# Optimization experiments

Measured on AMD Instinct MI355X. Metric: run time of the kernel, lower is better.

The kernel has to match this reference:

```python
import jax, jax.numpy as jnp
import numpy as np

KH = KW = 3
STRIDE, PAD, DIL = 1, 1, 1
HEADS, DG, CLIP, C = 12, 12, 2, 192
B, H, W = 4, 48, 48


def _linear_chw(x, w, b):
    # x: (n, d, c, h, w); Linear over channel dim (module rearranges to channels-last)
    return jnp.einsum('ndchw,oc->ndohw', x, w) + b[None, None, :, None, None]


def _deform_attn(q, kv, offset):
    # q: (b,1,C,H,W); kv: (b,clip,2C,H,W); offset: (b,clip,DG*K*2,H,W)
    b = q.shape[0]
    K = KH * KW
    HW = H * W
    dim = C // HEADS
    cg = 2 * C // DG  # channels per deformable group in kv (standard im2col split)
    ky = jnp.repeat(jnp.arange(KH), KW).astype(jnp.float32)  # (K,)
    kx = jnp.tile(jnp.arange(KW), KH).astype(jnp.float32)
    off = offset.reshape(b, CLIP, DG, K, 2, H, W)  # per-group [y,x] pairs per tap
    base_y = jnp.arange(H, dtype=jnp.float32)[None, :, None] * STRIDE - PAD + ky[:, None, None] * DIL  # (K,H,1)
    base_x = jnp.arange(W, dtype=jnp.float32)[None, None, :] * STRIDE - PAD + kx[:, None, None] * DIL  # (K,1,W)
    py = base_y + off[:, :, :, :, 0]  # (b,clip,dg,K,H,W)
    px = base_x + off[:, :, :, :, 1]
    kv_g = kv.reshape(b, CLIP, DG, cg, HW)

    y0 = jnp.floor(py)
    x0 = jnp.floor(px)
    wy1 = py - y0
    wx1 = px - x0

    def corner(yi, xi, wgt):
        valid = (yi >= 0) & (yi <= H - 1) & (xi >= 0) & (xi <= W - 1)
        idx = (jnp.clip(yi, 0, H - 1) * W + jnp.clip(xi, 0, W - 1)).astype(jnp.int32)
        idx = jnp.broadcast_to(idx.reshape(b, CLIP, DG, K, 1, HW), (b, CLIP, DG, K, cg, HW))
        src = jnp.broadcast_to(kv_g[:, :, :, None], (b, CLIP, DG, K, cg, HW))
        vals = jnp.take_along_axis(src, idx, axis=-1)  # gather over source pixels
        w_eff = (wgt * valid.astype(wgt.dtype)).reshape(b, CLIP, DG, K, 1, HW)
        return vals * w_eff

    s = (corner(y0, x0, (1 - wy1) * (1 - wx1))
         + corner(y0, x0 + 1, (1 - wy1) * wx1)
         + corner(y0 + 1, x0, wy1 * (1 - wx1))
         + corner(y0 + 1, x0 + 1, wy1 * wx1))  # (b,clip,dg,K,cg,HW)
    # restore channel order: (dg, cg) -> 2C = [C of k, C of v]
    s = s.transpose(0, 1, 2, 4, 3, 5).reshape(b, CLIP, 2, HEADS, dim, K, HW)
    ks, vs = s[:, :, 0], s[:, :, 1]  # (b,clip,heads,dim,K,HW)
    qh = q.reshape(b, HEADS, dim, HW) * (dim ** -0.5)
    scores = jnp.einsum('bhdn,bchdkn->bnhck', qh, ks)  # (b,HW,heads,clip,K)
    attn = jax.nn.softmax(scores.reshape(b, HW, HEADS, CLIP * K), axis=-1).reshape(b, HW, HEADS, CLIP, K)
    out = jnp.einsum('bnhck,bchdkn->bhdn', attn, vs)
    return out.reshape(b, 1, C, H, W)


def setup_inputs() -> dict:
    key = jax.random.key(0)
    ks = jax.random.split(key, 16)
    sd = 0.02
    return {
        'q': jax.random.normal(ks[0], (B, 1, C, H, W), jnp.float32),
        'k': jax.random.normal(ks[1], (B, CLIP, C, H, W), jnp.float32),
        'v': jax.random.normal(ks[2], (B, CLIP, C, H, W), jnp.float32),
        'offset': jax.random.normal(ks[3], (B, CLIP, DG * KH * KW * 2, H, W), jnp.float32),
        'wq': jax.random.normal(ks[4], (C, C), jnp.float32) * sd,
        'bq': jnp.zeros((C,), jnp.float32),
        'wk': jax.random.normal(ks[5], (C, C), jnp.float32) * sd,
        'bk': jnp.zeros((C,), jnp.float32),
        'wv': jax.random.normal(ks[6], (C, C), jnp.float32) * sd,
        'bv': jnp.zeros((C,), jnp.float32),
        'w1': jax.random.normal(ks[7], (2 * C, C), jnp.float32) * sd,
        'b1': jnp.zeros((2 * C,), jnp.float32),
        'w2': jax.random.normal(ks[8], (C, 2 * C), jnp.float32) * sd,
        'b2': jnp.zeros((C,), jnp.float32),
    }


def reference(q, k, v, offset, wq, bq, wk, bk, wv, bv, w1, b1, w2, b2):
    qp = _linear_chw(q, wq, bq)
    kv = jnp.concatenate([_linear_chw(k, wk, bk), _linear_chw(v, wv, bv)], axis=2)
    o = _deform_attn(qp, kv, offset)
    h = jnp.einsum('ndchw,oc->ndohw', o, w1) + b1[None, None, :, None, None]
    h = jax.nn.gelu(h, approximate=False)
    m = jnp.einsum('ndchw,oc->ndohw', h, w2) + b2[None, None, :, None, None]
    return o + m
```

## Files before the change

### kernel.cpp

```cpp
#include <hip/hip_runtime.h>

#define HW 2304
#define WID 48

typedef __attribute__((ext_vector_type(8))) short bf16x8;
typedef __attribute__((ext_vector_type(4))) float f32x4;
typedef __attribute__((ext_vector_type(2))) _Float16 half2v;

__device__ __forceinline__ half2v pk_h2(float lo, float hi) {
  return __builtin_bit_cast(half2v, __builtin_amdgcn_cvt_pkrtz(lo, hi));
}

__device__ __forceinline__ unsigned pack_bf2(float lo, float hi) {
  unsigned a = __builtin_bit_cast(unsigned, lo);
  unsigned b = __builtin_bit_cast(unsigned, hi);
  a = (a + 0x7FFFu + ((a >> 16) & 1u)) >> 16;
  b = (b + 0x7FFFu + ((b >> 16) & 1u)) >> 16;
  return a | (b << 16);
}
__device__ __forceinline__ unsigned short bf16_of(float x) {
  unsigned u = __builtin_bit_cast(unsigned, x);
  u = (u + 0x7FFFu + ((u >> 16) & 1u)) >> 16;
  return (unsigned short)u;
}
__device__ __forceinline__ unsigned short f16_of(float x) {
  _Float16 h = (_Float16)x;
  return __builtin_bit_cast(unsigned short, h);
}

__global__ __launch_bounds__(256) void prep_w(
    const float* __restrict__ wq, const float* __restrict__ wk,
    const float* __restrict__ wv, const float* __restrict__ w1,
    const float* __restrict__ w2, unsigned* __restrict__ wf)
{
  int fid = blockIdx.x * 4 + (threadIdx.x >> 6);
  int l = threadIdx.x & 63;
  const float* src; int K; int base;
  if (fid < 72)       { src = wq; K = 192; base = 0; }
  else if (fid < 144) { src = wk; K = 192; base = 72; }
  else if (fid < 216) { src = wv; K = 192; base = 144; }
  else if (fid < 360) { src = w1; K = 192; base = 216; }
  else                { src = w2; K = 384; base = 360; }
  int local = fid - base;
  int KS = K / 32;
  int nf = local / KS, ks = local % KS;
  int row = nf * 16 + (l & 15);
  int c0 = ks * 32 + (l >> 4) * 8;
  const float* p = src + (size_t)row * K + c0;
  float4 v0 = *(const float4*)p;
  float4 v1 = *(const float4*)(p + 4);
  unsigned* dst = wf + ((size_t)fid * 64 + l) * 4;
  dst[0] = pack_bf2(v0.x, v0.y);
  dst[1] = pack_bf2(v0.z, v0.w);
  dst[2] = pack_bf2(v1.x, v1.y);
  dst[3] = pack_bf2(v1.z, v1.w);
}

__global__ __launch_bounds__(256) void proj_mfma(
    const float* __restrict__ q, const float* __restrict__ k, const float* __restrict__ v,
    const unsigned* __restrict__ wf,
    const float* __restrict__ bq, const float* __restrict__ bk, const float* __restrict__ bv,
    float* __restrict__ qp, unsigned short* __restrict__ kvp)
{
  __shared__ unsigned lds[64 * 100];
  int slab = blockIdx.y;
  const float* in; const unsigned* wfr; const float* bias;
  float* outf = nullptr; unsigned short* outh = nullptr;
  if (slab < 4) {
    in = q + (size_t)slab * 192 * HW; wfr = wf; bias = bq;
    outf = qp + (size_t)slab * HW * 192;
  } else if (slab < 12) {
    int c = slab - 4;
    in = k + (size_t)c * 192 * HW; wfr = wf + 72 * 256; bias = bk;
    outh = kvp + (size_t)c * 2 * 6 * HW * 32;
  } else {
    int c = slab - 12;
    in = v + (size_t)c * 192 * HW; wfr = wf + 144 * 256; bias = bv;
    outh = kvp + ((size_t)c * 2 + 1) * 6 * HW * 32;
  }
  const int n0 = blockIdx.x * 64;
  const int t = threadIdx.x;
  const int w = t >> 6, l = t & 63;

  {
    int pix = t & 63;
    int cp0 = t >> 6;
    const float* s0 = in + n0 + pix;
#pragma unroll
    for (int i = 0; i < 24; ++i) {
      int cp = cp0 * 24 + i;
      float lo = s0[(size_t)(2 * cp) * HW];
      float hi = s0[(size_t)(2 * cp + 1) * HW];
      lds[pix * 100 + cp] = pack_bf2(lo, hi);
    }
  }

  bf16x8 wfrag[6][3];
#pragma unroll
  for (int ks = 0; ks < 6; ++ks)
#pragma unroll
    for (int nfi = 0; nfi < 3; ++nfi) {
      int nf = w * 3 + nfi;
      wfrag[ks][nfi] = ((const bf16x8*)wfr)[(nf * 6 + ks) * 64 + l];
    }

  __syncthreads();

  f32x4 acc[3][4];
#pragma unroll
  for (int a = 0; a < 3; ++a)
#pragma unroll
    for (int m = 0; m < 4; ++m) acc[a][m] = (f32x4){0.f, 0.f, 0.f, 0.f};

#pragma unroll
  for (int ks = 0; ks < 6; ++ks) {
    bf16x8 af[4];
#pragma unroll
    for (int mf = 0; mf < 4; ++mf)
      af[mf] = *(const bf16x8*)&lds[(mf * 16 + (l & 15)) * 100 + ks * 16 + (l >> 4) * 4];
#pragma unroll
    for (int nfi = 0; nfi < 3; ++nfi)
#pragma unroll
      for (int mf = 0; mf < 4; ++mf)
        acc[nfi][mf] = __builtin_amdgcn_mfma_f32_16x16x32_bf16(af[mf], wfrag[ks][nfi], acc[nfi][mf], 0, 0, 0);
  }

#pragma unroll
  for (int nfi = 0; nfi < 3; ++nfi) {
    int oc = (w * 3 + nfi) * 16 + (l & 15);
    float bs = bias[oc];
    if (outf) {
#pragma unroll
      for (int mf = 0; mf < 4; ++mf) {
        int pixb = n0 + mf * 16 + (l >> 4) * 4;
#pragma unroll
        for (int j = 0; j < 4; ++j)
          outf[(size_t)(pixb + j) * 192 + oc] = acc[nfi][mf][j] + bs;
      }
    } else {
      int pkh = oc >> 5, ch = oc & 31;
#pragma unroll
      for (int mf = 0; mf < 4; ++mf) {
        int pixb = n0 + mf * 16 + (l >> 4) * 4;
#pragma unroll
        for (int j = 0; j < 4; ++j)
          outh[((size_t)pkh * HW + pixb + j) * 32 + ch] = f16_of(acc[nfi][mf][j] + bs);
      }
    }
  }
}

__global__ __launch_bounds__(256, 4) void attn_kernel(
    const float* __restrict__ qp, const unsigned short* __restrict__ kvp,
    const float* __restrict__ offs, float* __restrict__ o_ws)
{
  __shared__ uint4 rec[2][2][9][32];
  const int t = threadIdx.x;
  const int g = blockIdx.x & 7;
  const int pos = blockIdx.x >> 3;
  const int b = g >> 1;
  const int half = g & 1;
  const int pk = pos / 36;
  const int tile = pos % 36;
  const int n_base = half * 1152 + tile * 32;

#pragma unroll
  for (int i = 0; i < 5; ++i) {
    int rid = t + i * 256;
    if (rid < 1152) {
      int rpix = rid & 31;
      int rest = rid >> 5;
      int rtap = rest % 9;
      int rq = rest / 9;
      int rclip = rq & 1;
      int dgsel = rq >> 1;
      int rn = n_base + rpix;
      int rh = rn / WID, rw = rn % WID;
      int dg = pk + dgsel * 6;
      const float* ob = offs + ((size_t)(b * 2 + rclip) * 216 + (size_t)(dg * 9 + rtap) * 2) * HW + rn;
      float oy = ob[0];
      float ox = ob[HW];
      float py = (float)(rh - 1 + rtap / 3) + oy;
      float px = (float)(rw - 1 + rtap % 3) + ox;
      float y0f = floorf(py), x0f = floorf(px);
      int y0 = (int)y0f, x0 = (int)x0f;
      float wy1 = py - y0f, wx1 = px - x0f;
      float wy0 = 1.f - wy1, wx0 = 1.f - wx1;
      unsigned ip[2];
      float wv[4];
#pragma unroll
      for (int cy = 0; cy < 2; ++cy) {
        int yi = y0 + cy;
        float wyv = cy ? wy1 : wy0;
        int yc = yi < 0 ? 0 : (yi > 47 ? 47 : yi);
        bool vy = (unsigned)yi < 48u;
#pragma unroll
        for (int cx = 0; cx < 2; ++cx) {
          int xi = x0 + cx;
          float wxv = cx ? wx1 : wx0;
          int xc = xi < 0 ? 0 : (xi > 47 ? 47 : xi);
          bool vx = (unsigned)xi < 48u;
          float wgt = (vy && vx) ? wyv * wxv : 0.f;
          int ci = cy * 2 + cx;
          wv[ci] = wgt;
          ((unsigned short*)ip)[ci] = (unsigned short)(yc * WID + xc);
        }
      }
      uint4 rc;
      rc.x = ip[0];
      rc.y = ip[1];
      rc.z = __builtin_bit_cast(unsigned, pk_h2(wv[0], wv[1]));
      rc.w = __builtin_bit_cast(unsigned, pk_h2(wv[2], wv[3]));
      rec[dgsel][rclip][rtap][rpix] = rc;
    }
  }

  const int l8 = t & 7;
  const int csel = l8 >> 2;
  const int chq = l8 & 3;
  const int pix = t >> 3;
  const int n = n_base + pix;

  half2v qh[4];
  {
    const float* qb = qp + ((size_t)b * HW + n) * 192 + pk * 32 + chq * 8;
    float4 v0 = *(const float4*)qb;
    float4 v1 = *(const float4*)(qb + 4);
    qh[0] = pk_h2(v0.x * 0.25f, v0.y * 0.25f);
    qh[1] = pk_h2(v0.z * 0.25f, v0.w * 0.25f);
    qh[2] = pk_h2(v1.x * 0.25f, v1.y * 0.25f);
    qh[3] = pk_h2(v1.z * 0.25f, v1.w * 0.25f);
  }

  __syncthreads();

  float sc[18];

#pragma unroll
  for (int c = 0; c < 2; ++c) {
    const unsigned short* kb = kvp + (((size_t)(b * 2 + c) * 2 + 0) * 6 + pk) * HW * 32 + chq * 8;
#pragma unroll
    for (int kk = 0; kk < 9; ++kk) {
      uint4 rc = rec[0][c][kk][pix];
      float s = 0.f;
#pragma unroll
      for (int r = 0; r < 2; ++r) {
        unsigned pr = r ? rc.y : rc.x;
        unsigned idx = csel ? (pr >> 16) : (pr & 0xFFFFu);
        half2v wp = __builtin_bit_cast(half2v, r ? rc.w : rc.z);
        _Float16 wh = csel ? wp.y : wp.x;
        uint4 u = *(const uint4*)(kb + (size_t)idx * 32);
        float d = __builtin_amdgcn_fdot2(qh[0], __builtin_bit_cast(half2v, u.x), 0.f, false);
        d = __builtin_amdgcn_fdot2(qh[1], __builtin_bit_cast(half2v, u.y), d, false);
        d = __builtin_amdgcn_fdot2(qh[2], __builtin_bit_cast(half2v, u.z), d, false);
        d = __builtin_amdgcn_fdot2(qh[3], __builtin_bit_cast(half2v, u.w), d, false);
        s += (float)wh * d;
      }
      sc[c * 9 + kk] = s;
    }
  }

#pragma unroll
  for (int j = 0; j < 18; ++j) sc[j] += __shfl_xor(sc[j], 1, 64);
#pragma unroll
  for (int j = 0; j < 18; ++j) sc[j] += __shfl_xor(sc[j], 4, 64);

  {
    float m = -1e30f;
#pragma unroll
    for (int j = 0; j < 18; ++j) m = fmaxf(m, sc[j]);
    float sum = 0.f;
#pragma unroll
    for (int j = 0; j < 18; ++j) { float ev = __expf(sc[j] - m); sc[j] = ev; sum += ev; }
    float inv = 1.f / sum;
#pragma unroll
    for (int j = 0; j < 18; ++j) sc[j] *= inv;
  }

  float acc[8];
#pragma unroll
  for (int i = 0; i < 8; ++i) acc[i] = 0.f;
#pragma unroll
  for (int c = 0; c < 2; ++c) {
    const unsigned short* vb = kvp + (((size_t)(b * 2 + c) * 2 + 1) * 6 + pk) * HW * 32 + chq * 8;
#pragma unroll
    for (int kk = 0; kk < 9; ++kk) {
      uint4 rc = rec[1][c][kk][pix];
      float at = sc[c * 9 + kk];
#pragma unroll
      for (int r = 0; r < 2; ++r) {
        unsigned pr = r ? rc.y : rc.x;
        unsigned idx = csel ? (pr >> 16) : (pr & 0xFFFFu);
        half2v wp = __builtin_bit_cast(half2v, r ? rc.w : rc.z);
        _Float16 wh = csel ? wp.y : wp.x;
        uint4 u = *(const uint4*)(vb + (size_t)idx * 32);
        float cw = (float)wh * at;
        half2v v0 = __builtin_bit_cast(half2v, u.x);
        half2v v1 = __builtin_bit_cast(half2v, u.y);
        half2v v2 = __builtin_bit_cast(half2v, u.z);
        half2v v3 = __builtin_bit_cast(half2v, u.w);
        acc[0] += cw * (float)v0.x; acc[1] += cw * (float)v0.y;
        acc[2] += cw * (float)v1.x; acc[3] += cw * (float)v1.y;
        acc[4] += cw * (float)v2.x; acc[5] += cw * (float)v2.y;
        acc[6] += cw * (float)v3.x; acc[7] += cw * (float)v3.y;
      }
    }
  }

#pragma unroll
  for (int i = 0; i < 8; ++i) acc[i] += __shfl_xor(acc[i], 4, 64);

  if (csel == 0) {
    float* orow = o_ws + ((size_t)b * HW + n) * 192 + pk * 32 + chq * 8;
    float4 r0; r0.x = acc[0]; r0.y = acc[1]; r0.z = acc[2]; r0.w = acc[3];
    float4 r1; r1.x = acc[4]; r1.y = acc[5]; r1.z = acc[6]; r1.w = acc[7];
    *(float4*)orow = r0;
    *(float4*)(orow + 4) = r1;
  }
}

__global__ __launch_bounds__(256) void mlp_mfma(
    const float* __restrict__ o_ws, const unsigned* __restrict__ wf,
    const float* __restrict__ b1, const float* __restrict__ b2,
    float* __restrict__ out)
{
  __shared__ unsigned ldsO[16 * 100];
  __shared__ unsigned ldsH[16 * 196];
  const unsigned* w1f = wf + 216 * 256;
  const unsigned* w2f = wf + 360 * 256;
  const int blk = blockIdx.x;
  const int b = blk / 144;
  const int n0 = (blk % 144) * 16;
  const int t = threadIdx.x;
  const int w = t >> 6, l = t & 63;

  for (int i = t; i < 16 * 96; i += 256) {
    int pix = i / 96, cp = i % 96;
    const float2 s = *(const float2*)(o_ws + ((size_t)(b * HW) + n0 + pix) * 192 + 2 * cp);
    ldsO[pix * 100 + cp] = pack_bf2(s.x, s.y);
  }
  __syncthreads();

  f32x4 acc1[6];
#pragma unroll
  for (int a = 0; a < 6; ++a) acc1[a] = (f32x4){0.f, 0.f, 0.f, 0.f};
#pragma unroll
  for (int ks = 0; ks < 6; ++ks) {
    bf16x8 af = *(const bf16x8*)&ldsO[(l & 15) * 100 + ks * 16 + (l >> 4) * 4];
#pragma unroll
    for (int nfi = 0; nfi < 6; ++nfi) {
      int nf = w * 6 + nfi;
      bf16x8 bfr = ((const bf16x8*)w1f)[(nf * 6 + ks) * 64 + l];
      acc1[nfi] = __builtin_amdgcn_mfma_f32_16x16x32_bf16(af, bfr, acc1[nfi], 0, 0, 0);
    }
  }

  {
    unsigned short* ldsHu = (unsigned short*)ldsH;
#pragma unroll
    for (int nfi = 0; nfi < 6; ++nfi) {
      int hc = (w * 6 + nfi) * 16 + (l & 15);
      float bs = b1[hc];
#pragma unroll
      for (int j = 0; j < 4; ++j) {
        int pix = (l >> 4) * 4 + j;
        float x = acc1[nfi][j] + bs;
        float gl = 0.5f * x * (1.f + erff(x * 0.70710678118654752f));
        ldsHu[pix * 392 + hc] = bf16_of(gl);
      }
    }
  }
  __syncthreads();

  f32x4 acc2[3];
#pragma unroll
  for (int a = 0; a < 3; ++a) acc2[a] = (f32x4){0.f, 0.f, 0.f, 0.f};
#pragma unroll
  for (int ks = 0; ks < 12; ++ks) {
    bf16x8 af = *(const bf16x8*)&ldsH[(l & 15) * 196 + ks * 16 + (l >> 4) * 4];
#pragma unroll
    for (int nfi = 0; nfi < 3; ++nfi) {
      int nf = w * 3 + nfi;
      bf16x8 bfr = ((const bf16x8*)w2f)[(nf * 12 + ks) * 64 + l];
      acc2[nfi] = __builtin_amdgcn_mfma_f32_16x16x32_bf16(af, bfr, acc2[nfi], 0, 0, 0);
    }
  }

#pragma unroll
  for (int nfi = 0; nfi < 3; ++nfi) {
    int oc = (w * 3 + nfi) * 16 + (l & 15);
    float bs = b2[oc];
#pragma unroll
    for (int j = 0; j < 4; ++j) {
      int pix = (l >> 4) * 4 + j;
      float res = o_ws[((size_t)(b * HW) + n0 + pix) * 192 + oc];
      out[((size_t)b * 192 + oc) * HW + n0 + pix] = acc2[nfi][j] + bs + res;
    }
  }
}

extern "C" void kernel_launch(void* const* d_in, const int* in_sizes, int n_in,
                              void* d_out, int out_size, void* d_ws, size_t ws_size,
                              hipStream_t stream) {
  const float* q = (const float*)d_in[0];
  const float* k = (const float*)d_in[1];
  const float* v = (const float*)d_in[2];
  const float* offset = (const float*)d_in[3];
  const float* wq = (const float*)d_in[4];
  const float* bq = (const float*)d_in[5];
  const float* wk = (const float*)d_in[6];
  const float* bk = (const float*)d_in[7];
  const float* wv = (const float*)d_in[8];
  const float* bv = (const float*)d_in[9];
  const float* w1 = (const float*)d_in[10];
  const float* b1 = (const float*)d_in[11];
  const float* w2 = (const float*)d_in[12];
  const float* b2 = (const float*)d_in[13];
  float* out = (float*)d_out;

  float* qp_t = (float*)d_ws;
  float* o_ws = qp_t + (size_t)4 * HW * 192;
  unsigned short* kvp = (unsigned short*)(o_ws + (size_t)4 * HW * 192);
  unsigned* wfb = (unsigned*)(kvp + (size_t)8 * 2 * 6 * HW * 32);

  prep_w<<<dim3(126), dim3(256), 0, stream>>>(wq, wk, wv, w1, w2, wfb);
  proj_mfma<<<dim3(36, 20), dim3(256), 0, stream>>>(q, k, v, wfb, bq, bk, bv, qp_t, kvp);
  attn_kernel<<<dim3(1728), dim3(256), 0, stream>>>(qp_t, kvp, offset, o_ws);
  mlp_mfma<<<dim3(576), dim3(256), 0, stream>>>(o_ws, wfb, b1, b2, out);
}
```

Baseline: 64.37 us.

## Split deformable attention across clips with flash-style partial softmax combine

The attention kernel now handles one clip per block, doubling the grid. Each block writes unnormalized outputs along with its running max and sum to a partial buffer. A new combine kernel merges the two clip partials using log-sum-exp rescaling and writes the normalized output. This adds parallelism and cuts per-block register and LDS use, at the cost of an extra kernel launch and a round trip of partial results through global memory.

```diff
diff --git a/kernel.cpp b/kernel.cpp
--- a/kernel.cpp
+++ b/kernel.cpp
@@ -150,34 +150,35 @@
   }
 }
 
-__global__ __launch_bounds__(256, 4) void attn_kernel(
+__global__ __launch_bounds__(256, 4) void attn_part(
     const float* __restrict__ qp, const unsigned short* __restrict__ kvp,
-    const float* __restrict__ offs, float* __restrict__ o_ws)
+    const float* __restrict__ offs, float* __restrict__ opart)
 {
-  __shared__ uint4 rec[2][2][9][32];
+  __shared__ uint4 rec[2][9][32];
   const int t = threadIdx.x;
   const int g = blockIdx.x & 7;
   const int pos = blockIdx.x >> 3;
   const int b = g >> 1;
   const int half = g & 1;
-  const int pk = pos / 36;
-  const int tile = pos % 36;
+  const int clip = pos / 216;
+  const int r2 = pos % 216;
+  const int pk = r2 / 36;
+  const int tile = r2 % 36;
   const int n_base = half * 1152 + tile * 32;
-
-#pragma unroll
-  for (int i = 0; i < 5; ++i) {
+  const int bc = b * 2 + clip;
+
+#pragma unroll
+  for (int i = 0; i < 3; ++i) {
     int rid = t + i * 256;
-    if (rid < 1152) {
+    if (rid < 576) {
       int rpix = rid & 31;
       int rest = rid >> 5;
       int rtap = rest % 9;
-      int rq = rest / 9;
-      int rclip = rq & 1;
-      int dgsel = rq >> 1;
+      int dgsel = rest / 9;
       int rn = n_base + rpix;
       int rh = rn / WID, rw = rn % WID;
       int dg = pk + dgsel * 6;
-      const float* ob = offs + ((size_t)(b * 2 + rclip) * 216 + (size_t)(dg * 9 + rtap) * 2) * HW + rn;
+      const float* ob = offs + ((size_t)bc * 216 + (size_t)(dg * 9 + rtap) * 2) * HW + rn;
       float oy = ob[0];
       float ox = ob[HW];
       float py = (float)(rh - 1 + rtap / 3) + oy;
@@ -211,7 +212,7 @@
       rc.y = ip[1];
       rc.z = __builtin_bit_cast(unsigned, pk_h2(wv[0], wv[1]));
       rc.w = __builtin_bit_cast(unsigned, pk_h2(wv[2], wv[3]));
-      rec[dgsel][rclip][rtap][rpix] = rc;
+      rec[dgsel][rtap][rpix] = rc;
     }
   }
 
@@ -234,14 +235,13 @@
 
   __syncthreads();
 
-  float sc[18];
-
-#pragma unroll
-  for (int c = 0; c < 2; ++c) {
-    const unsigned short* kb = kvp + (((size_t)(b * 2 + c) * 2 + 0) * 6 + pk) * HW * 32 + chq * 8;
+  float sc[9];
+
+  {
+    const unsigned short* kb = kvp + (((size_t)bc * 2 + 0) * 6 + pk) * HW * 32 + chq * 8;
 #pragma unroll
     for (int kk = 0; kk < 9; ++kk) {
-      uint4 rc = rec[0][c][kk][pix];
+      uint4 rc = rec[0][kk][pix];
       float s = 0.f;
 #pragma unroll
       for (int r = 0; r < 2; ++r) {
@@ -256,37 +256,31 @@
         d = __builtin_amdgcn_fdot2(qh[3], __builtin_bit_cast(half2v, u.w), d, false);
         s += (float)wh * d;
       }
-      sc[c * 9 + kk] = s;
-    }
-  }
-
-#pragma unroll
-  for (int j = 0; j < 18; ++j) sc[j] += __shfl_xor(sc[j], 1, 64);
-#pragma unroll
-  for (int j = 0; j < 18; ++j) sc[j] += __shfl_xor(sc[j], 4, 64);
-
+      sc[kk] = s;
+    }
+  }
+
+#pragma unroll
+  for (int j = 0; j < 9; ++j) sc[j] += __shfl_xor(sc[j], 1, 64);
+#pragma unroll
+  for (int j = 0; j < 9; ++j) sc[j] += __shfl_xor(sc[j], 4, 64);
+
+  float m = -1e30f;
+#pragma unroll
+  for (int j = 0; j < 9; ++j) m = fmaxf(m, sc[j]);
+  float Z = 0.f;
+#pragma unroll
+  for (int j = 0; j < 9; ++j) { float ev = __expf(sc[j] - m); sc[j] = ev; Z += ev; }
+
+  float acc[8];
+#pragma unroll
+  for (int i = 0; i < 8; ++i) acc[i] = 0.f;
   {
-    float m = -1e30f;
-#pragma unroll
-    for (int j = 0; j < 18; ++j) m = fmaxf(m, sc[j]);
-    float sum = 0.f;
-#pragma unroll
-    for (int j = 0; j < 18; ++j) { float ev = __expf(sc[j] - m); sc[j] = ev; sum += ev; }
-    float inv = 1.f / sum;
-#pragma unroll
-    for (int j = 0; j < 18; ++j) sc[j] *= inv;
-  }
-
-  float acc[8];
-#pragma unroll
-  for (int i = 0; i < 8; ++i) acc[i] = 0.f;
-#pragma unroll
-  for (int c = 0; c < 2; ++c) {
-    const unsigned short* vb = kvp + (((size_t)(b * 2 + c) * 2 + 1) * 6 + pk) * HW * 32 + chq * 8;
+    const unsigned short* vb = kvp + (((size_t)bc * 2 + 1) * 6 + pk) * HW * 32 + chq * 8;
 #pragma unroll
     for (int kk = 0; kk < 9; ++kk) {
-      uint4 rc = rec[1][c][kk][pix];
-      float at = sc[c * 9 + kk];
+      uint4 rc = rec[1][kk][pix];
+      float at = sc[kk];
 #pragma unroll
       for (int r = 0; r < 2; ++r) {
         unsigned pr = r ? rc.y : rc.x;
@@ -311,12 +305,46 @@
   for (int i = 0; i < 8; ++i) acc[i] += __shfl_xor(acc[i], 4, 64);
 
   if (csel == 0) {
-    float* orow = o_ws + ((size_t)b * HW + n) * 192 + pk * 32 + chq * 8;
+    float* obase = opart + ((((size_t)clip * 4 + b) * 6 + pk) * HW + n) * 36;
     float4 r0; r0.x = acc[0]; r0.y = acc[1]; r0.z = acc[2]; r0.w = acc[3];
     float4 r1; r1.x = acc[4]; r1.y = acc[5]; r1.z = acc[6]; r1.w = acc[7];
-    *(float4*)orow = r0;
-    *(float4*)(orow + 4) = r1;
-  }
+    *(float4*)(obase + chq * 8) = r0;
+    *(float4*)(obase + chq * 8 + 4) = r1;
+    if (chq == 0) { obase[32] = m; obase[33] = Z; }
+    if (chq == 2) { obase[34] = m; obase[35] = Z; }
+  }
+}
+
+__global__ __launch_bounds__(256) void attn_combine(
+    const float* __restrict__ opart, float* __restrict__ o_ws)
+{
+  int gid = blockIdx.x * 256 + threadIdx.x;
+  int chq = gid & 3;
+  int e = gid >> 2;
+  int n = e % HW;
+  int r = e / HW;
+  int pk = r % 6;
+  int b = r / 6;
+  const float* pa = opart + (((size_t)(b * 6 + pk)) * HW + n) * 36;
+  const float* pb = pa + (size_t)24 * HW * 36;
+  int hsel = chq >> 1;
+  float ma = pa[32 + 2 * hsel], za = pa[33 + 2 * hsel];
+  float mb = pb[32 + 2 * hsel], zb = pb[33 + 2 * hsel];
+  float m = fmaxf(ma, mb);
+  float sa = __expf(ma - m), sb = __expf(mb - m);
+  float inv = 1.f / (za * sa + zb * sb);
+  float4 a0 = *(const float4*)(pa + chq * 8);
+  float4 a1 = *(const float4*)(pa + chq * 8 + 4);
+  float4 b0 = *(const float4*)(pb + chq * 8);
+  float4 b1 = *(const float4*)(pb + chq * 8 + 4);
+  float* o = o_ws + ((size_t)b * HW + n) * 192 + pk * 32 + chq * 8;
+  float4 r0, r1;
+  r0.x = (a0.x * sa + b0.x * sb) * inv; r0.y = (a0.y * sa + b0.y * sb) * inv;
+  r0.z = (a0.z * sa + b0.z * sb) * inv; r0.w = (a0.w * sa + b0.w * sb) * inv;
+  r1.x = (a1.x * sa + b1.x * sb) * inv; r1.y = (a1.y * sa + b1.y * sb) * inv;
+  r1.z = (a1.z * sa + b1.z * sb) * inv; r1.w = (a1.w * sa + b1.w * sb) * inv;
+  *(float4*)o = r0;
+  *(float4*)(o + 4) = r1;
 }
 
 __global__ __launch_bounds__(256) void mlp_mfma(
@@ -422,9 +450,11 @@
   float* o_ws = qp_t + (size_t)4 * HW * 192;
   unsigned short* kvp = (unsigned short*)(o_ws + (size_t)4 * HW * 192);
   unsigned* wfb = (unsigned*)(kvp + (size_t)8 * 2 * 6 * HW * 32);
+  float* opart = (float*)(wfb + 504 * 256);
 
   prep_w<<<dim3(126), dim3(256), 0, stream>>>(wq, wk, wv, w1, w2, wfb);
   proj_mfma<<<dim3(36, 20), dim3(256), 0, stream>>>(q, k, v, wfb, bq, bk, bv, qp_t, kvp);
-  attn_kernel<<<dim3(1728), dim3(256), 0, stream>>>(qp_t, kvp, offset, o_ws);
+  attn_part<<<dim3(3456), dim3(256), 0, stream>>>(qp_t, kvp, offset, opart);
+  attn_combine<<<dim3(864), dim3(256), 0, stream>>>(opart, o_ws);
   mlp_mfma<<<dim3(576), dim3(256), 0, stream>>>(o_ws, wfb, b1, b2, out);
 }
```

Result: slower. 70.68 us (+9.8%).

## Stage a row window of K/V planes in shared memory for deformable gathers

Applied to the files above, without the earlier changes.

Each attention block now copies a band of up to 13 rows of the current K or V plane (per clip) into a ~39KB LDS buffer. Gathers that land inside the window read from LDS, and those outside fall back to global memory. This removes scattered global/L2 gather latency, at the cost of bulk copies, four extra barriers, and lower occupancy (launch bounds drop from 4 to 2 blocks). Most of the copied window may go unused, since each block only reads 32 pixels times 9 taps.

```diff
diff --git a/kernel.cpp b/kernel.cpp
--- a/kernel.cpp
+++ b/kernel.cpp
@@ -150,11 +150,12 @@
   }
 }
 
-__global__ __launch_bounds__(256, 4) void attn_kernel(
+__global__ __launch_bounds__(256, 2) void attn_kernel(
     const float* __restrict__ qp, const unsigned short* __restrict__ kvp,
     const float* __restrict__ offs, float* __restrict__ o_ws)
 {
   __shared__ uint4 rec[2][2][9][32];
+  __shared__ unsigned short win[624 * 32];
   const int t = threadIdx.x;
   const int g = blockIdx.x & 7;
   const int pos = blockIdx.x >> 3;
@@ -163,6 +164,13 @@
   const int pk = pos / 36;
   const int tile = pos % 36;
   const int n_base = half * 1152 + tile * 32;
+
+  const int hh_lo = n_base / WID;
+  const int hh_hi = (n_base + 31) / WID;
+  int wlo = hh_lo - 5; if (wlo < 0) wlo = 0;
+  int whi = hh_hi + 6; if (whi > 47) whi = 47;
+  const unsigned wlo48 = (unsigned)(wlo * WID);
+  const unsigned wlen = (unsigned)((whi - wlo + 1) * WID);
 
 #pragma unroll
   for (int i = 0; i < 5; ++i) {
@@ -232,13 +240,17 @@
     qh[3] = pk_h2(v1.z * 0.25f, v1.w * 0.25f);
   }
 
-  __syncthreads();
-
   float sc[18];
 
-#pragma unroll
   for (int c = 0; c < 2; ++c) {
-    const unsigned short* kb = kvp + (((size_t)(b * 2 + c) * 2 + 0) * 6 + pk) * HW * 32 + chq * 8;
+    const unsigned short* kplane = kvp + (((size_t)(b * 2 + c) * 2 + 0) * 6 + pk) * HW * 32;
+    {
+      const uint4* src4 = (const uint4*)(kplane + (size_t)wlo48 * 32);
+      uint4* dst4 = (uint4*)win;
+      for (int i = t; i < (int)(wlen * 4); i += 256) dst4[i] = src4[i];
+    }
+    __syncthreads();
+    const unsigned short* kb = kplane + chq * 8;
 #pragma unroll
     for (int kk = 0; kk < 9; ++kk) {
       uint4 rc = rec[0][c][kk][pix];
@@ -249,7 +261,10 @@
         unsigned idx = csel ? (pr >> 16) : (pr & 0xFFFFu);
         half2v wp = __builtin_bit_cast(half2v, r ? rc.w : rc.z);
         _Float16 wh = csel ? wp.y : wp.x;
-        uint4 u = *(const uint4*)(kb + (size_t)idx * 32);
+        unsigned rel = idx - wlo48;
+        uint4 u;
+        if (rel < wlen) u = *(const uint4*)(win + rel * 32 + chq * 8);
+        else            u = *(const uint4*)(kb + (size_t)idx * 32);
         float d = __builtin_amdgcn_fdot2(qh[0], __builtin_bit_cast(half2v, u.x), 0.f, false);
         d = __builtin_amdgcn_fdot2(qh[1], __builtin_bit_cast(half2v, u.y), d, false);
         d = __builtin_amdgcn_fdot2(qh[2], __builtin_bit_cast(half2v, u.z), d, false);
@@ -258,6 +273,7 @@
       }
       sc[c * 9 + kk] = s;
     }
+    __syncthreads();
   }
 
 #pragma unroll
@@ -280,9 +296,15 @@
   float acc[8];
 #pragma unroll
   for (int i = 0; i < 8; ++i) acc[i] = 0.f;
-#pragma unroll
   for (int c = 0; c < 2; ++c) {
-    const unsigned short* vb = kvp + (((size_t)(b * 2 + c) * 2 + 1) * 6 + pk) * HW * 32 + chq * 8;
+    const unsigned short* vplane = kvp + (((size_t)(b * 2 + c) * 2 + 1) * 6 + pk) * HW * 32;
+    {
+      const uint4* src4 = (const uint4*)(vplane + (size_t)wlo48 * 32);
+      uint4* dst4 = (uint4*)win;
+      for (int i = t; i < (int)(wlen * 4); i += 256) dst4[i] = src4[i];
+    }
+    __syncthreads();
+    const unsigned short* vb = vplane + chq * 8;
 #pragma unroll
     for (int kk = 0; kk < 9; ++kk) {
       uint4 rc = rec[1][c][kk][pix];
@@ -293,7 +315,10 @@
         unsigned idx = csel ? (pr >> 16) : (pr & 0xFFFFu);
         half2v wp = __builtin_bit_cast(half2v, r ? rc.w : rc.z);
         _Float16 wh = csel ? wp.y : wp.x;
-        uint4 u = *(const uint4*)(vb + (size_t)idx * 32);
+        unsigned rel = idx - wlo48;
+        uint4 u;
+        if (rel < wlen) u = *(const uint4*)(win + rel * 32 + chq * 8);
+        else            u = *(const uint4*)(vb + (size_t)idx * 32);
         float cw = (float)wh * at;
         half2v v0 = __builtin_bit_cast(half2v, u.x);
         half2v v1 = __builtin_bit_cast(half2v, u.y);
@@ -305,6 +330,7 @@
         acc[6] += cw * (float)v3.x; acc[7] += cw * (float)v3.y;
       }
     }
+    __syncthreads();
   }
 
 #pragma unroll
```

New measurement: 103.8 us. 61.2% more time.
